# Optimization experiments

Measured on AMD Instinct MI355X. Metric: run time of the kernel, lower is better.

Reference implementation:

```python
import jax, jax.numpy as jnp
import numpy as np

B, S, D, H = 2, 1024, 2048, 16
NOPE, ROPE, VD, KVR, QLR = 128, 64, 128, 512, 1536
NE, TOPK, MI, SMI = 16, 2, 1408, 2816
QKD = NOPE + ROPE
SCALE = QKD ** -0.5
EPS = 1e-3


def _rms(x, w):
    return w * (x * jax.lax.rsqrt(jnp.mean(x * x, axis=-1, keepdims=True) + EPS))


def _lin(x, w, b):
    return x @ w.T + b


def _rope(x, cos, sin):
    # x: (B,S,H,dr); cos/sin: (S, dr//2); consecutive-pair complex rotation as in torch view_as_complex
    xs = x.reshape(*x.shape[:-1], -1, 2)
    x0, x1 = xs[..., 0], xs[..., 1]
    c = cos[None, :, None, :]
    s = sin[None, :, None, :]
    y = jnp.stack([x0 * c - x1 * s, x0 * s + x1 * c], axis=-1)
    return y.reshape(x.shape)


def setup_inputs() -> dict:
    ks = iter(jax.random.split(jax.random.key(0), 64))

    def w(*shape):
        return jax.random.normal(next(ks), shape, jnp.float32) * 0.02

    ang = jnp.arange(S)[:, None] * (1.0 / (10000.0 ** (jnp.arange(0, ROPE, 2) / ROPE)))[None, :]
    return {
        "x": jax.random.normal(next(ks), (B, S, D), jnp.float32),
        "attn_norm_w": jnp.ones(D, jnp.float32),
        "ffn_norm_w": jnp.ones(D, jnp.float32),
        "wq_a_w": w(QLR, D), "wq_a_b": w(QLR),
        "q_norm_w": jnp.ones(QLR, jnp.float32),
        "wq_b_w": w(H * QKD, QLR), "wq_b_b": w(H * QKD),
        "wkv_a_w": w(KVR + ROPE, D), "wkv_a_b": w(KVR + ROPE),
        "kv_norm_w": jnp.ones(KVR, jnp.float32),
        "wkv_b_w": w(H * (NOPE + VD), KVR),
        "wo_w": w(D, H * VD), "wo_b": w(D),
        "gate_w": w(NE, D), "gate_b": w(NE),
        "e_w1": w(NE, MI, D), "e_b1": w(NE, MI),
        "e_w2": w(NE, D, MI), "e_b2": w(NE, D),
        "e_w3": w(NE, MI, D), "e_b3": w(NE, MI),
        "s_w1": w(SMI, D), "s_b1": w(SMI),
        "s_w2": w(D, SMI), "s_b2": w(D),
        "s_w3": w(SMI, D), "s_b3": w(SMI),
        "cos": jnp.cos(ang), "sin": jnp.sin(ang),
        "start_pos": 0,
    }


def _forward(x, attn_norm_w, ffn_norm_w, wq_a_w, wq_a_b, q_norm_w, wq_b_w, wq_b_b,
             wkv_a_w, wkv_a_b, kv_norm_w, wkv_b_w, wo_w, wo_b,
             gate_w, gate_b, e_w1, e_b1, e_w2, e_b2, e_w3, e_b3,
             s_w1, s_b1, s_w2, s_b2, s_w3, s_b3, cos, sin, start_pos):
    # ---------------- MLA attention ----------------
    h = _rms(x, attn_norm_w)
    q = _lin(_rms(_lin(h, wq_a_w, wq_a_b), q_norm_w), wq_b_w, wq_b_b).reshape(B, S, H, QKD)
    q_nope, q_pe = q[..., :NOPE], q[..., NOPE:]
    q_pe = _rope(q_pe, cos, sin)
    kvf = _lin(h, wkv_a_w, wkv_a_b)
    kv, k_pe = kvf[..., :KVR], kvf[..., KVR:]
    k_pe = _rope(k_pe[:, :, None, :], cos, sin)[:, :, 0, :]          # (B,S,ROPE)
    wb = wkv_b_w.reshape(H, NOPE + VD, KVR)
    q_abs = jnp.einsum('bshd,hdc->bshc', q_nope, wb[:, :NOPE])       # absorbed q (B,S,H,KVR)
    kv_n = _rms(kv, kv_norm_w)                                       # kv cache content, start_pos=0
    scores = (jnp.einsum('bshc,btc->bsht', q_abs, kv_n)
              + jnp.einsum('bshr,btr->bsht', q_pe, k_pe)) * SCALE
    # NOTE: source constructs a causal mask but never applies it -> full attention (faithful)
    p = jax.nn.softmax(scores.astype(jnp.float32), axis=-1).astype(x.dtype)
    o = jnp.einsum('bsht,btc->bshc', p, kv_n)
    o = jnp.einsum('bshc,hdc->bshd', o, wb[:, NOPE:])
    x = x + _lin(o.reshape(B, S, H * VD), wo_w, wo_b)
    # ---------------- MoE FFN ----------------
    h2 = _rms(x, ffn_norm_w).reshape(-1, D)                          # (T,D)
    probs = jax.nn.softmax((h2 @ gate_w.T + gate_b).astype(jnp.float32), axis=-1)
    _, idx = jax.lax.top_k(probs + gate_b, TOPK)                     # bias re-added post-softmax, as in source
    wts = jnp.take_along_axis(probs, idx, axis=-1).astype(x.dtype)   # route_scale = 1.0
    T = h2.shape[0]
    combine = jnp.zeros((T, NE), x.dtype).at[jnp.arange(T)[:, None], idx].add(wts)
    a = jnp.einsum('td,eid->tei', h2, e_w1) + e_b1
    g = jax.nn.silu(a) * (jnp.einsum('td,eid->tei', h2, e_w3) + e_b3)
    gm = g * combine[:, :, None]
    y = jnp.einsum('tei,edi->td', gm, e_w2) + combine @ e_b2
    z = _lin(jax.nn.silu(_lin(h2, s_w1, s_b1)) * _lin(h2, s_w3, s_b3), s_w2, s_b2)
    return x + (y + z + h2).reshape(B, S, D)


def reference(x, attn_norm_w, ffn_norm_w, wq_a_w, wq_a_b, q_norm_w, wq_b_w, wq_b_b,
              wkv_a_w, wkv_a_b, kv_norm_w, wkv_b_w, wo_w, wo_b,
              gate_w, gate_b, e_w1, e_b1, e_w2, e_b2, e_w3, e_b3,
              s_w1, s_b1, s_w2, s_b2, s_w3, s_b3, cos, sin, start_pos):
    return _forward(x, attn_norm_w, ffn_norm_w, wq_a_w, wq_a_b, q_norm_w, wq_b_w, wq_b_b,
                    wkv_a_w, wkv_a_b, kv_norm_w, wkv_b_w, wo_w, wo_b,
                    gate_w, gate_b, e_w1, e_b1, e_w2, e_b2, e_w3, e_b3,
                    s_w1, s_b1, s_w2, s_b2, s_w3, s_b3, cos, sin, start_pos)
```

## Files before the change

### kernel.cpp

```cpp
#include <hip/hip_runtime.h>
#include <math.h>

constexpr int B_ = 2, S_ = 1024, D_ = 2048, H_ = 16;
constexpr int NOPE_ = 128, ROPE_ = 64, VD_ = 128, KVR_ = 512, QLR_ = 1536;
constexpr int NE_ = 16, MI_ = 1408, SMI_ = 2816;
constexpr int QKD_ = NOPE_ + ROPE_;
constexpr int T_ = B_ * S_;
constexpr float SCALE_ = 0.07216878364870322f;
constexpr float EPS_ = 1e-3f;
constexpr int MAX_TILES_ = 80;

typedef __attribute__((ext_vector_type(8))) short  bf16x8_t;
typedef __attribute__((ext_vector_type(4))) float  f32x4_t;
typedef __attribute__((ext_vector_type(4))) unsigned short us4_t;

__device__ __forceinline__ void split_bf(float v, unsigned short& h, unsigned short& l)
{
    unsigned int u = __float_as_uint(v);
    unsigned short hb = (unsigned short)((u + 0x7FFFu + ((u >> 16) & 1u)) >> 16);
    float hf = __uint_as_float((unsigned int)hb << 16);
    float lo = v - hf;
    unsigned int u2 = __float_as_uint(lo);
    l = (unsigned short)((u2 + 0x7FFFu + ((u2 >> 16) & 1u)) >> 16);
    h = hb;
}

__global__ __launch_bounds__(256) void gemm_mfma_kernel(
    const float* __restrict__ A, int lda, long strideA,
    const float* __restrict__ W, int ldw, long strideW, int w_kn,
    const float* __restrict__ bias, long strideBias,
    const float* __restrict__ res, int ldr, long strideRes,
    float* __restrict__ C, int ldc, long strideC,
    int M, int N, int K)
{
    (void)M; (void)N;
    const int bz = blockIdx.z;
    A += (long)bz * strideA;
    W += (long)bz * strideW;
    C += (long)bz * strideC;
    if (bias) bias += (long)bz * strideBias;
    if (res)  res  += (long)bz * strideRes;

    __shared__ unsigned short Ah[128][40], Al[128][40];
    __shared__ unsigned short Bh[128][40], Bl[128][40];

    const int m0 = blockIdx.y * 128;
    const int n0 = blockIdx.x * 128;
    const int tid  = threadIdx.x;
    const int lane = tid & 63;
    const int wv   = tid >> 6;
    const int wm = (wv >> 1) * 64, wn = (wv & 1) * 64;
    const int r16 = lane & 15, g4 = lane >> 4;

    f32x4_t acc[4][4];
    #pragma unroll
    for (int i = 0; i < 4; i++)
        #pragma unroll
        for (int j = 0; j < 4; j++) acc[i][j] = (f32x4_t){0.f, 0.f, 0.f, 0.f};

    const int sr   = tid >> 3;
    const int scol = (tid & 7) * 4;
    const int tcol = tid & 63, tkr = tid >> 6;

    for (int kt = 0; kt < K; kt += 32) {
        #pragma unroll
        for (int rr = 0; rr < 128; rr += 32) {
            const float4 v = *(const float4*)(A + (long)(m0 + rr + sr) * lda + (kt + scol));
            us4_t h, l;
            split_bf(v.x, ((unsigned short*)&h)[0], ((unsigned short*)&l)[0]);
            split_bf(v.y, ((unsigned short*)&h)[1], ((unsigned short*)&l)[1]);
            split_bf(v.z, ((unsigned short*)&h)[2], ((unsigned short*)&l)[2]);
            split_bf(v.w, ((unsigned short*)&h)[3], ((unsigned short*)&l)[3]);
            *(us4_t*)&Ah[rr + sr][scol] = h;
            *(us4_t*)&Al[rr + sr][scol] = l;
        }
        if (w_kn == 0) {
            #pragma unroll
            for (int rr = 0; rr < 128; rr += 32) {
                const float4 v = *(const float4*)(W + (long)(n0 + rr + sr) * ldw + (kt + scol));
                us4_t h, l;
                split_bf(v.x, ((unsigned short*)&h)[0], ((unsigned short*)&l)[0]);
                split_bf(v.y, ((unsigned short*)&h)[1], ((unsigned short*)&l)[1]);
                split_bf(v.z, ((unsigned short*)&h)[2], ((unsigned short*)&l)[2]);
                split_bf(v.w, ((unsigned short*)&h)[3], ((unsigned short*)&l)[3]);
                *(us4_t*)&Bh[rr + sr][scol] = h;
                *(us4_t*)&Bl[rr + sr][scol] = l;
            }
        } else {
            #pragma unroll
            for (int cb = 0; cb < 128; cb += 64)
                #pragma unroll
                for (int kb = 0; kb < 32; kb += 4) {
                    float v = W[(long)(kt + kb + tkr) * ldw + (n0 + cb + tcol)];
                    unsigned short h, l;
                    split_bf(v, h, l);
                    Bh[cb + tcol][kb + tkr] = h;
                    Bl[cb + tcol][kb + tkr] = l;
                }
        }
        __syncthreads();

        bf16x8_t ah[4], al[4], bh[4], bl[4];
        #pragma unroll
        for (int i = 0; i < 4; i++) {
            ah[i] = *(const bf16x8_t*)&Ah[wm + i * 16 + r16][g4 * 8];
            al[i] = *(const bf16x8_t*)&Al[wm + i * 16 + r16][g4 * 8];
            bh[i] = *(const bf16x8_t*)&Bh[wn + i * 16 + r16][g4 * 8];
            bl[i] = *(const bf16x8_t*)&Bl[wn + i * 16 + r16][g4 * 8];
        }
        #pragma unroll
        for (int i = 0; i < 4; i++)
            #pragma unroll
            for (int j = 0; j < 4; j++) {
                f32x4_t t = acc[i][j];
                t = __builtin_amdgcn_mfma_f32_16x16x32_bf16(ah[i], bh[j], t, 0, 0, 0);
                t = __builtin_amdgcn_mfma_f32_16x16x32_bf16(ah[i], bl[j], t, 0, 0, 0);
                t = __builtin_amdgcn_mfma_f32_16x16x32_bf16(al[i], bh[j], t, 0, 0, 0);
                acc[i][j] = t;
            }
        __syncthreads();
    }

    #pragma unroll
    for (int i = 0; i < 4; i++)
        #pragma unroll
        for (int rr = 0; rr < 4; rr++) {
            const int m = m0 + wm + i * 16 + g4 * 4 + rr;
            #pragma unroll
            for (int j = 0; j < 4; j++) {
                const int n = n0 + wn + j * 16 + r16;
                float v = acc[i][j][rr];
                if (bias) v += bias[n];
                if (res)  v += res[(long)m * ldr + n];
                C[(long)m * ldc + n] = v;
            }
        }
}

__global__ __launch_bounds__(256) void gemm_kernel(
    const float* __restrict__ A, int lda, long strideA,
    const float* __restrict__ W, int ldw, long strideW, int w_kn,
    const float* __restrict__ bias, long strideBias,
    const float* __restrict__ res, int ldr, long strideRes,
    float* __restrict__ C, int ldc, long strideC,
    int M, int N, int K)
{
    (void)M;
    const int bz = blockIdx.z;
    A += (long)bz * strideA;
    W += (long)bz * strideW;
    C += (long)bz * strideC;
    if (bias) bias += (long)bz * strideBias;
    if (res)  res  += (long)bz * strideRes;

    __shared__ float As[16][68];
    __shared__ float Ws[16][68];

    const int m0 = blockIdx.y * 64;
    const int n0 = blockIdx.x * 64;
    const int tid = threadIdx.x;
    const int tx = tid & 15;
    const int ty = tid >> 4;

    float acc[4][4] = {};

    for (int kt = 0; kt < K; kt += 16) {
        #pragma unroll
        for (int i = 0; i < 4; i++) {
            int p = tid + i * 256;
            int r = p >> 4, kk = p & 15;
            As[kk][r] = A[(long)(m0 + r) * lda + (kt + kk)];
        }
        if (w_kn) {
            #pragma unroll
            for (int i = 0; i < 4; i++) {
                int p = tid + i * 256;
                int kk = p >> 6, n = p & 63;
                Ws[kk][n] = W[(long)(kt + kk) * ldw + (n0 + n)];
            }
        } else {
            #pragma unroll
            for (int i = 0; i < 4; i++) {
                int p = tid + i * 256;
                int n = p >> 4, kk = p & 15;
                Ws[kk][n] = W[(long)(n0 + n) * ldw + (kt + kk)];
            }
        }
        __syncthreads();
        #pragma unroll
        for (int kk = 0; kk < 16; kk++) {
            float a[4], b[4];
            #pragma unroll
            for (int i = 0; i < 4; i++) a[i] = As[kk][ty * 4 + i];
            #pragma unroll
            for (int j = 0; j < 4; j++) b[j] = Ws[kk][tx * 4 + j];
            #pragma unroll
            for (int i = 0; i < 4; i++)
                #pragma unroll
                for (int j = 0; j < 4; j++)
                    acc[i][j] += a[i] * b[j];
        }
        __syncthreads();
    }

    #pragma unroll
    for (int i = 0; i < 4; i++) {
        int m = m0 + ty * 4 + i;
        #pragma unroll
        for (int j = 0; j < 4; j++) {
            int n = n0 + tx * 4 + j;
            float v = acc[i][j];
            if (bias) v += bias[n];
            if (res)  v += res[(long)m * ldr + n];
            C[(long)m * ldc + n] = v;
        }
    }
}

__global__ __launch_bounds__(256) void rms_kernel(
    const float* __restrict__ in, float* __restrict__ out,
    const float* __restrict__ w, int N, int in_stride, int out_stride)
{
    const int row = blockIdx.x;
    const float* x = in + (long)row * in_stride;
    float* y = out + (long)row * out_stride;
    __shared__ float red[256];
    const int tid = threadIdx.x;
    float s = 0.f;
    for (int i = tid; i < N; i += 256) { float v = x[i]; s += v * v; }
    red[tid] = s; __syncthreads();
    for (int st = 128; st > 0; st >>= 1) {
        if (tid < st) red[tid] += red[tid + st];
        __syncthreads();
    }
    const float scale = rsqrtf(red[0] / (float)N + EPS_);
    for (int i = tid; i < N; i += 256) y[i] = w[i] * x[i] * scale;
}

__global__ void rope_kernel(float* __restrict__ p,
                            const float* __restrict__ cosb,
                            const float* __restrict__ sinb,
                            int nheads, int row_stride, int head_stride,
                            int off, int total)
{
    int i = blockIdx.x * 256 + threadIdx.x;
    if (i >= total) return;
    int pair = i & 31;
    int rem = i >> 5;
    int h = rem % nheads;
    int t = rem / nheads;
    int s = t % S_;
    float c = cosb[s * 32 + pair], sn = sinb[s * 32 + pair];
    float* base = p + (long)t * row_stride + (long)h * head_stride + off + pair * 2;
    float x0 = base[0], x1 = base[1];
    base[0] = x0 * c - x1 * sn;
    base[1] = x0 * sn + x1 * c;
}

__global__ __launch_bounds__(256) void softmax_kernel(float* __restrict__ sc)
{
    float* row = sc + (long)blockIdx.x * 1024;
    const int tid = threadIdx.x;
    __shared__ float red[256];

    float4 v = ((const float4*)row)[tid];
    v.x *= SCALE_; v.y *= SCALE_; v.z *= SCALE_; v.w *= SCALE_;

    float m = fmaxf(fmaxf(v.x, v.y), fmaxf(v.z, v.w));
    red[tid] = m; __syncthreads();
    for (int st = 128; st > 0; st >>= 1) {
        if (tid < st) red[tid] = fmaxf(red[tid], red[tid + st]);
        __syncthreads();
    }
    m = red[0];
    __syncthreads();

    v.x = __expf(v.x - m); v.y = __expf(v.y - m);
    v.z = __expf(v.z - m); v.w = __expf(v.w - m);
    float s = v.x + v.y + v.z + v.w;
    red[tid] = s; __syncthreads();
    for (int st = 128; st > 0; st >>= 1) {
        if (tid < st) red[tid] += red[tid + st];
        __syncthreads();
    }
    const float inv = 1.f / red[0];

    v.x *= inv; v.y *= inv; v.z *= inv; v.w *= inv;
    ((float4*)row)[tid] = v;
}

__global__ __launch_bounds__(256) void gate_kernel(
    const float* __restrict__ h2, const float* __restrict__ gw,
    const float* __restrict__ gb, int* __restrict__ idx,
    float* __restrict__ wts)
{
    const int t = blockIdx.x;
    __shared__ float red[256];
    __shared__ float logits[16];
    const int tid = threadIdx.x;
    const int e = tid >> 4, lane = tid & 15;
    const float* x = h2 + (long)t * 2048;
    float s = 0.f;
    for (int i = lane; i < 2048; i += 16) s += x[i] * gw[e * 2048 + i];
    red[tid] = s; __syncthreads();
    for (int st = 8; st > 0; st >>= 1) {
        if (lane < st) red[tid] += red[tid + st];
        __syncthreads();
    }
    if (lane == 0) logits[e] = red[e * 16] + gb[e];
    __syncthreads();
    if (tid == 0) {
        float m = logits[0];
        for (int j = 1; j < 16; j++) m = fmaxf(m, logits[j]);
        float pr[16]; float sum = 0.f;
        for (int j = 0; j < 16; j++) { pr[j] = expf(logits[j] - m); sum += pr[j]; }
        float inv = 1.f / sum;
        for (int j = 0; j < 16; j++) pr[j] *= inv;
        int i1 = 0; float v1 = -1e30f;
        for (int j = 0; j < 16; j++) { float v = pr[j] + gb[j]; if (v > v1) { v1 = v; i1 = j; } }
        int i2 = 0; float v2 = -1e30f;
        for (int j = 0; j < 16; j++) { if (j == i1) continue; float v = pr[j] + gb[j]; if (v > v2) { v2 = v; i2 = j; } }
        idx[t * 2 + 0] = i1; idx[t * 2 + 1] = i2;
        wts[t * 2 + 0] = pr[i1]; wts[t * 2 + 1] = pr[i2];
    }
}

__global__ __launch_bounds__(256) void route_kernel(
    const int* __restrict__ idx, const float* __restrict__ wts,
    int* __restrict__ slot_te, float* __restrict__ slot_w,
    int* __restrict__ tile_e, int* __restrict__ tile_row0,
    int* __restrict__ tile_cnt, int* __restrict__ n_tiles)
{
    __shared__ int counts[16], offs[16], cursor[16];
    const int tid = threadIdx.x;
    if (tid < 16) { counts[tid] = 0; cursor[tid] = 0; }
    __syncthreads();
    for (int a = tid; a < 2 * T_; a += 256) atomicAdd(&counts[idx[a]], 1);
    __syncthreads();
    if (tid == 0) {
        int o = 0;
        for (int e = 0; e < 16; e++) { offs[e] = o; o += counts[e]; }
        int nt = 0;
        for (int e = 0; e < 16; e++) {
            for (int r0 = 0; r0 < counts[e]; r0 += 64) {
                tile_e[nt] = e;
                tile_row0[nt] = offs[e] + r0;
                int c = counts[e] - r0;
                tile_cnt[nt] = c < 64 ? c : 64;
                nt++;
            }
        }
        *n_tiles = nt;
    }
    __syncthreads();
    for (int a = tid; a < 2 * T_; a += 256) {
        int e = idx[a];
        int pos = offs[e] + atomicAdd(&cursor[e], 1);
        int t = a >> 1, k = a & 1;
        slot_te[pos * 2 + 0] = (t << 1) | k;
        slot_te[pos * 2 + 1] = e;
        slot_w[pos] = wts[a];
    }
}

__global__ __launch_bounds__(256) void moe_mlp13_kernel(
    const float* __restrict__ h2,
    const int* __restrict__ slot_te,
    const int* __restrict__ tile_e, const int* __restrict__ tile_row0,
    const int* __restrict__ tile_cnt, const int* __restrict__ n_tiles,
    const float* __restrict__ w1, const float* __restrict__ b1,
    const float* __restrict__ w3, const float* __restrict__ b3,
    float* __restrict__ G)
{
    const int tile = blockIdx.y;
    if (tile >= *n_tiles) return;
    const int e    = tile_e[tile];
    const int row0 = tile_row0[tile];
    const int tcnt = tile_cnt[tile];
    const int n0   = blockIdx.x * 128;

    __shared__ unsigned short Ah[64][40],  Al[64][40];
    __shared__ unsigned short B1h[128][40], B1l[128][40];
    __shared__ unsigned short B3h[128][40], B3l[128][40];
    __shared__ int tok[64];

    const int tid  = threadIdx.x;
    const int lane = tid & 63;
    const int wv   = tid >> 6;
    const int r16 = lane & 15, g4 = lane >> 4;

    if (tid < 64) {
        int r = tid < tcnt ? tid : tcnt - 1;
        tok[tid] = slot_te[(row0 + r) * 2 + 0] >> 1;
    }
    __syncthreads();

    const float* W1 = w1 + (long)e * MI_ * 2048;
    const float* W3 = w3 + (long)e * MI_ * 2048;

    f32x4_t acc1[4][2], acc3[4][2];
    #pragma unroll
    for (int i = 0; i < 4; i++)
        #pragma unroll
        for (int j = 0; j < 2; j++) {
            acc1[i][j] = (f32x4_t){0.f, 0.f, 0.f, 0.f};
            acc3[i][j] = (f32x4_t){0.f, 0.f, 0.f, 0.f};
        }

    const int sr   = tid >> 3;
    const int scol = (tid & 7) * 4;

    for (int kt = 0; kt < 2048; kt += 32) {
        #pragma unroll
        for (int rr = 0; rr < 64; rr += 32) {
            const float4 v = *(const float4*)(h2 + (long)tok[rr + sr] * 2048 + (kt + scol));
            us4_t h, l;
            split_bf(v.x, ((unsigned short*)&h)[0], ((unsigned short*)&l)[0]);
            split_bf(v.y, ((unsigned short*)&h)[1], ((unsigned short*)&l)[1]);
            split_bf(v.z, ((unsigned short*)&h)[2], ((unsigned short*)&l)[2]);
            split_bf(v.w, ((unsigned short*)&h)[3], ((unsigned short*)&l)[3]);
            *(us4_t*)&Ah[rr + sr][scol] = h;
            *(us4_t*)&Al[rr + sr][scol] = l;
        }
        #pragma unroll
        for (int rr = 0; rr < 128; rr += 32) {
            const long woff = (long)(n0 + rr + sr) * 2048 + (kt + scol);
            {
                const float4 v = *(const float4*)(W1 + woff);
                us4_t h, l;
                split_bf(v.x, ((unsigned short*)&h)[0], ((unsigned short*)&l)[0]);
                split_bf(v.y, ((unsigned short*)&h)[1], ((unsigned short*)&l)[1]);
                split_bf(v.z, ((unsigned short*)&h)[2], ((unsigned short*)&l)[2]);
                split_bf(v.w, ((unsigned short*)&h)[3], ((unsigned short*)&l)[3]);
                *(us4_t*)&B1h[rr + sr][scol] = h;
                *(us4_t*)&B1l[rr + sr][scol] = l;
            }
            {
                const float4 v = *(const float4*)(W3 + woff);
                us4_t h, l;
                split_bf(v.x, ((unsigned short*)&h)[0], ((unsigned short*)&l)[0]);
                split_bf(v.y, ((unsigned short*)&h)[1], ((unsigned short*)&l)[1]);
                split_bf(v.z, ((unsigned short*)&h)[2], ((unsigned short*)&l)[2]);
                split_bf(v.w, ((unsigned short*)&h)[3], ((unsigned short*)&l)[3]);
                *(us4_t*)&B3h[rr + sr][scol] = h;
                *(us4_t*)&B3l[rr + sr][scol] = l;
            }
        }
        __syncthreads();

        bf16x8_t ah[4], al[4], b1h[2], b1l[2], b3h[2], b3l[2];
        #pragma unroll
        for (int i = 0; i < 4; i++) {
            ah[i] = *(const bf16x8_t*)&Ah[i * 16 + r16][g4 * 8];
            al[i] = *(const bf16x8_t*)&Al[i * 16 + r16][g4 * 8];
        }
        #pragma unroll
        for (int j = 0; j < 2; j++) {
            const int cn = wv * 32 + j * 16 + r16;
            b1h[j] = *(const bf16x8_t*)&B1h[cn][g4 * 8];
            b1l[j] = *(const bf16x8_t*)&B1l[cn][g4 * 8];
            b3h[j] = *(const bf16x8_t*)&B3h[cn][g4 * 8];
            b3l[j] = *(const bf16x8_t*)&B3l[cn][g4 * 8];
        }
        #pragma unroll
        for (int i = 0; i < 4; i++)
            #pragma unroll
            for (int j = 0; j < 2; j++) {
                f32x4_t t = acc1[i][j];
                t = __builtin_amdgcn_mfma_f32_16x16x32_bf16(ah[i], b1h[j], t, 0, 0, 0);
                t = __builtin_amdgcn_mfma_f32_16x16x32_bf16(ah[i], b1l[j], t, 0, 0, 0);
                t = __builtin_amdgcn_mfma_f32_16x16x32_bf16(al[i], b1h[j], t, 0, 0, 0);
                acc1[i][j] = t;
                f32x4_t u = acc3[i][j];
                u = __builtin_amdgcn_mfma_f32_16x16x32_bf16(ah[i], b3h[j], u, 0, 0, 0);
                u = __builtin_amdgcn_mfma_f32_16x16x32_bf16(ah[i], b3l[j], u, 0, 0, 0);
                u = __builtin_amdgcn_mfma_f32_16x16x32_bf16(al[i], b3h[j], u, 0, 0, 0);
                acc3[i][j] = u;
            }
        __syncthreads();
    }

    #pragma unroll
    for (int i = 0; i < 4; i++)
        #pragma unroll
        for (int rr = 0; rr < 4; rr++) {
            const int rl = i * 16 + g4 * 4 + rr;
            if (rl >= tcnt) continue;
            const long grow = (long)(row0 + rl) * MI_;
            #pragma unroll
            for (int j = 0; j < 2; j++) {
                const int n = n0 + wv * 32 + j * 16 + r16;
                float a = acc1[i][j][rr] + b1[e * MI_ + n];
                float b = acc3[i][j][rr] + b3[e * MI_ + n];
                G[grow + n] = (a / (1.f + expf(-a))) * b;
            }
        }
}

__global__ __launch_bounds__(256) void moe_mlp2_kernel(
    const float* __restrict__ G,
    const int* __restrict__ slot_te, const float* __restrict__ slot_w,
    const int* __restrict__ tile_e, const int* __restrict__ tile_row0,
    const int* __restrict__ tile_cnt, const int* __restrict__ n_tiles,
    const float* __restrict__ w2, const float* __restrict__ b2,
    float* __restrict__ y0, float* __restrict__ y1)
{
    const int tile = blockIdx.y;
    if (tile >= *n_tiles) return;
    const int e    = tile_e[tile];
    const int row0 = tile_row0[tile];
    const int tcnt = tile_cnt[tile];
    const int n0   = blockIdx.x * 128;

    __shared__ unsigned short Ah[64][40], Al[64][40];
    __shared__ unsigned short Bh[128][40], Bl[128][40];
    __shared__ int rsrc[64];

    const int tid  = threadIdx.x;
    const int lane = tid & 63;
    const int wv   = tid >> 6;
    const int r16 = lane & 15, g4 = lane >> 4;

    if (tid < 64) {
        int r = tid < tcnt ? tid : tcnt - 1;
        rsrc[tid] = row0 + r;
    }
    __syncthreads();

    const float* W2 = w2 + (long)e * 2048 * MI_;

    f32x4_t acc[4][2];
    #pragma unroll
    for (int i = 0; i < 4; i++)
        #pragma unroll
        for (int j = 0; j < 2; j++) acc[i][j] = (f32x4_t){0.f, 0.f, 0.f, 0.f};

    const int sr   = tid >> 3;
    const int scol = (tid & 7) * 4;

    for (int kt = 0; kt < MI_; kt += 32) {
        #pragma unroll
        for (int rr = 0; rr < 64; rr += 32) {
            const float4 v = *(const float4*)(G + (long)rsrc[rr + sr] * MI_ + (kt + scol));
            us4_t h, l;
            split_bf(v.x, ((unsigned short*)&h)[0], ((unsigned short*)&l)[0]);
            split_bf(v.y, ((unsigned short*)&h)[1], ((unsigned short*)&l)[1]);
            split_bf(v.z, ((unsigned short*)&h)[2], ((unsigned short*)&l)[2]);
            split_bf(v.w, ((unsigned short*)&h)[3], ((unsigned short*)&l)[3]);
            *(us4_t*)&Ah[rr + sr][scol] = h;
            *(us4_t*)&Al[rr + sr][scol] = l;
        }
        #pragma unroll
        for (int rr = 0; rr < 128; rr += 32) {
            const float4 v = *(const float4*)(W2 + (long)(n0 + rr + sr) * MI_ + (kt + scol));
            us4_t h, l;
            split_bf(v.x, ((unsigned short*)&h)[0], ((unsigned short*)&l)[0]);
            split_bf(v.y, ((unsigned short*)&h)[1], ((unsigned short*)&l)[1]);
            split_bf(v.z, ((unsigned short*)&h)[2], ((unsigned short*)&l)[2]);
            split_bf(v.w, ((unsigned short*)&h)[3], ((unsigned short*)&l)[3]);
            *(us4_t*)&Bh[rr + sr][scol] = h;
            *(us4_t*)&Bl[rr + sr][scol] = l;
        }
        __syncthreads();

        bf16x8_t ah[4], al[4], bh[2], bl[2];
        #pragma unroll
        for (int i = 0; i < 4; i++) {
            ah[i] = *(const bf16x8_t*)&Ah[i * 16 + r16][g4 * 8];
            al[i] = *(const bf16x8_t*)&Al[i * 16 + r16][g4 * 8];
        }
        #pragma unroll
        for (int j = 0; j < 2; j++) {
            const int cn = wv * 32 + j * 16 + r16;
            bh[j] = *(const bf16x8_t*)&Bh[cn][g4 * 8];
            bl[j] = *(const bf16x8_t*)&Bl[cn][g4 * 8];
        }
        #pragma unroll
        for (int i = 0; i < 4; i++)
            #pragma unroll
            for (int j = 0; j < 2; j++) {
                f32x4_t t = acc[i][j];
                t = __builtin_amdgcn_mfma_f32_16x16x32_bf16(ah[i], bh[j], t, 0, 0, 0);
                t = __builtin_amdgcn_mfma_f32_16x16x32_bf16(ah[i], bl[j], t, 0, 0, 0);
                t = __builtin_amdgcn_mfma_f32_16x16x32_bf16(al[i], bh[j], t, 0, 0, 0);
                acc[i][j] = t;
            }
        __syncthreads();
    }

    #pragma unroll
    for (int i = 0; i < 4; i++)
        #pragma unroll
        for (int rr = 0; rr < 4; rr++) {
            const int rl = i * 16 + g4 * 4 + rr;
            if (rl >= tcnt) continue;
            const int slot = row0 + rl;
            const int tk = slot_te[slot * 2 + 0];
            const int t = tk >> 1, k = tk & 1;
            const float wgt = slot_w[slot];
            float* y = (k ? y1 : y0) + (long)t * 2048;
            #pragma unroll
            for (int j = 0; j < 2; j++) {
                const int n = n0 + wv * 32 + j * 16 + r16;
                y[n] = wgt * (acc[i][j][rr] + b2[e * 2048 + n]);
            }
        }
}

__global__ void silu_mul_kernel(float* __restrict__ u1,
                                const float* __restrict__ u3, long n)
{
    long i = (long)blockIdx.x * 256 + threadIdx.x;
    if (i >= n) return;
    float a = u1[i];
    u1[i] = (a / (1.f + expf(-a))) * u3[i];
}

__global__ void final_add_kernel(const float* __restrict__ x2,
                                 const float* __restrict__ h2,
                                 const float* __restrict__ y0,
                                 const float* __restrict__ y1,
                                 const float* __restrict__ z,
                                 float* __restrict__ out, long n)
{
    long i = (long)blockIdx.x * 256 + threadIdx.x;
    if (i >= n) return;
    out[i] = x2[i] + h2[i] + y0[i] + y1[i] + z[i];
}

extern "C" void kernel_launch(void* const* d_in, const int* in_sizes, int n_in,
                              void* d_out, int out_size, void* d_ws, size_t ws_size,
                              hipStream_t stream)
{
    (void)in_sizes; (void)n_in; (void)out_size; (void)ws_size;

    const float* x          = (const float*)d_in[0];
    const float* attn_nw    = (const float*)d_in[1];
    const float* ffn_nw     = (const float*)d_in[2];
    const float* wq_a_w     = (const float*)d_in[3];
    const float* wq_a_b     = (const float*)d_in[4];
    const float* q_norm_w   = (const float*)d_in[5];
    const float* wq_b_w     = (const float*)d_in[6];
    const float* wq_b_b     = (const float*)d_in[7];
    const float* wkv_a_w    = (const float*)d_in[8];
    const float* wkv_a_b    = (const float*)d_in[9];
    const float* kv_norm_w  = (const float*)d_in[10];
    const float* wkv_b_w    = (const float*)d_in[11];
    const float* wo_w       = (const float*)d_in[12];
    const float* wo_b       = (const float*)d_in[13];
    const float* gate_w     = (const float*)d_in[14];
    const float* gate_b     = (const float*)d_in[15];
    const float* e_w1       = (const float*)d_in[16];
    const float* e_b1       = (const float*)d_in[17];
    const float* e_w2       = (const float*)d_in[18];
    const float* e_b2       = (const float*)d_in[19];
    const float* e_w3       = (const float*)d_in[20];
    const float* e_b3       = (const float*)d_in[21];
    const float* s_w1       = (const float*)d_in[22];
    const float* s_b1       = (const float*)d_in[23];
    const float* s_w2       = (const float*)d_in[24];
    const float* s_b2       = (const float*)d_in[25];
    const float* s_w3       = (const float*)d_in[26];
    const float* s_b3       = (const float*)d_in[27];
    const float* cosb       = (const float*)d_in[28];
    const float* sinb       = (const float*)d_in[29];

    float* ws = (float*)d_ws;
    float* h    = ws + 0;
    float* qa   = ws + 4194304;
    float* q    = ws + 7340032;
    float* kvf  = ws + 13631488;
    float* qabs = ws + 14811136;
    float* o2   = ws + 31588352;
    float* x2   = ws + 35782656;
    float* h2   = ws + 39976960;
    float* u1   = ws + 44171264;
    float* u3   = ws + 49938432;
    float* wts  = ws + 55705600;
    int*   idx  = (int*)(ws + 55709696);
    int*   slot_te = (int*)(ws + 55713792);
    float* slot_w  = ws + 55721984;
    float* y0 = h;
    float* y1 = q;
    float* z  = u3;

    float* scores = o2;

    float* G = qabs;
    int* tile_e    = (int*)(qabs + 5767168);
    int* tile_row0 = tile_e + MAX_TILES_;
    int* tile_cnt  = tile_e + 2 * MAX_TILES_;
    int* n_tiles   = tile_e + 3 * MAX_TILES_;

    rms_kernel<<<dim3(T_), 256, 0, stream>>>(x, h, attn_nw, 2048, 2048, 2048);

    gemm_mfma_kernel<<<dim3(QLR_ / 128, T_ / 128, 1), 256, 0, stream>>>(
        h, 2048, 0, wq_a_w, 2048, 0, 0, wq_a_b, 0,
        nullptr, 0, 0, qa, QLR_, 0, T_, QLR_, 2048);

    rms_kernel<<<dim3(T_), 256, 0, stream>>>(qa, qa, q_norm_w, QLR_, QLR_, QLR_);

    gemm_mfma_kernel<<<dim3(H_ * QKD_ / 128, T_ / 128, 1), 256, 0, stream>>>(
        qa, QLR_, 0, wq_b_w, QLR_, 0, 0, wq_b_b, 0,
        nullptr, 0, 0, q, H_ * QKD_, 0, T_, H_ * QKD_, QLR_);

    gemm_kernel<<<dim3((KVR_ + ROPE_) / 64, T_ / 64, 1), 256, 0, stream>>>(
        h, 2048, 0, wkv_a_w, 2048, 0, 0, wkv_a_b, 0,
        nullptr, 0, 0, kvf, KVR_ + ROPE_, 0, T_, KVR_ + ROPE_, 2048);

    {
        int total_q = T_ * H_ * 32;
        rope_kernel<<<dim3((total_q + 255) / 256), 256, 0, stream>>>(
            q, cosb, sinb, H_, H_ * QKD_, QKD_, NOPE_, total_q);
        int total_k = T_ * 32;
        rope_kernel<<<dim3((total_k + 255) / 256), 256, 0, stream>>>(
            kvf, cosb, sinb, 1, KVR_ + ROPE_, 0, KVR_, total_k);
    }

    rms_kernel<<<dim3(T_), 256, 0, stream>>>(kvf, kvf, kv_norm_w, KVR_,
                                             KVR_ + ROPE_, KVR_ + ROPE_);

    gemm_mfma_kernel<<<dim3(KVR_ / 128, T_ / 128, H_), 256, 0, stream>>>(
        q, H_ * QKD_, QKD_,
        wkv_b_w, KVR_, (long)256 * KVR_, 1,
        nullptr, 0, nullptr, 0, 0,
        qabs, H_ * KVR_, KVR_, T_, KVR_, NOPE_);

    for (int b = 0; b < B_; b++) {
        const float* kvb = kvf + (long)b * S_ * (KVR_ + ROPE_);
        gemm_mfma_kernel<<<dim3(S_ / 128, S_ / 128, H_), 256, 0, stream>>>(
            qabs + (long)b * S_ * H_ * KVR_, H_ * KVR_, KVR_,
            kvb, KVR_ + ROPE_, 0, 0,
            nullptr, 0, nullptr, 0, 0,
            scores, S_, (long)S_ * S_, S_, S_, KVR_);
        gemm_mfma_kernel<<<dim3(S_ / 128, S_ / 128, H_), 256, 0, stream>>>(
            q + (long)b * S_ * H_ * QKD_ + NOPE_, H_ * QKD_, QKD_,
            kvb + KVR_, KVR_ + ROPE_, 0, 0,
            nullptr, 0, scores, S_, (long)S_ * S_,
            scores, S_, (long)S_ * S_, S_, S_, ROPE_);
        softmax_kernel<<<dim3(H_ * S_), 256, 0, stream>>>(scores);
        gemm_mfma_kernel<<<dim3(KVR_ / 128, S_ / 128, H_), 256, 0, stream>>>(
            scores, S_, (long)S_ * S_,
            kvb, KVR_ + ROPE_, 0, 1,
            nullptr, 0, nullptr, 0, 0,
            qabs + (long)b * S_ * H_ * KVR_, H_ * KVR_, KVR_, S_, KVR_, S_);
    }

    gemm_mfma_kernel<<<dim3(VD_ / 128, T_ / 128, H_), 256, 0, stream>>>(
        qabs, H_ * KVR_, KVR_,
        wkv_b_w + (long)NOPE_ * KVR_, KVR_, (long)256 * KVR_, 0,
        nullptr, 0, nullptr, 0, 0,
        o2, H_ * VD_, VD_, T_, VD_, KVR_);

    gemm_mfma_kernel<<<dim3(D_ / 128, T_ / 128, 1), 256, 0, stream>>>(
        o2, 2048, 0, wo_w, 2048, 0, 0, wo_b, 0,
        x, 2048, 0, x2, 2048, 0, T_, D_, 2048);

    rms_kernel<<<dim3(T_), 256, 0, stream>>>(x2, h2, ffn_nw, 2048, 2048, 2048);

    gate_kernel<<<dim3(T_), 256, 0, stream>>>(h2, gate_w, gate_b, idx, wts);

    route_kernel<<<dim3(1), 256, 0, stream>>>(idx, wts, slot_te, slot_w,
                                              tile_e, tile_row0, tile_cnt, n_tiles);

    moe_mlp13_kernel<<<dim3(MI_ / 128, MAX_TILES_), 256, 0, stream>>>(
        h2, slot_te, tile_e, tile_row0, tile_cnt, n_tiles,
        e_w1, e_b1, e_w3, e_b3, G);
    moe_mlp2_kernel<<<dim3(D_ / 128, MAX_TILES_), 256, 0, stream>>>(
        G, slot_te, slot_w, tile_e, tile_row0, tile_cnt, n_tiles,
        e_w2, e_b2, y0, y1);

    gemm_mfma_kernel<<<dim3(SMI_ / 128, T_ / 128, 1), 256, 0, stream>>>(
        h2, 2048, 0, s_w1, 2048, 0, 0, s_b1, 0,
        nullptr, 0, 0, u1, SMI_, 0, T_, SMI_, 2048);
    gemm_mfma_kernel<<<dim3(SMI_ / 128, T_ / 128, 1), 256, 0, stream>>>(
        h2, 2048, 0, s_w3, 2048, 0, 0, s_b3, 0,
        nullptr, 0, 0, u3, SMI_, 0, T_, SMI_, 2048);
    {
        long n = (long)T_ * SMI_;
        silu_mul_kernel<<<dim3((unsigned)((n + 255) / 256)), 256, 0, stream>>>(u1, u3, n);
    }
    gemm_mfma_kernel<<<dim3(D_ / 128, T_ / 128, 1), 256, 0, stream>>>(
        u1, SMI_, 0, s_w2, SMI_, 0, 0, s_b2, 0,
        nullptr, 0, 0, z, D_, 0, T_, D_, SMI_);

    {
        long n = (long)T_ * D_;
        final_add_kernel<<<dim3((unsigned)((n + 255) / 256)), 256, 0, stream>>>(
            x2, h2, y0, y1, z, (float*)d_out, n);
    }
}
```

Measured before the change: 2.740 ms.

## Fuse rope-score GEMM, silu-mul epilogue, MFMA kv_a GEMM, truncating bf16 split

Adds a second K-segment (A2/W2) to the MFMA GEMM so the nope and rope score products are computed in one launch instead of a separate accumulate pass. The silu-mul elementwise kernel is folded into the w3 GEMM epilogue, and the wkv_a projection moves from the scalar fp32 GEMM to the MFMA kernel with an N-limit clamp. The bf16 hi/lo split now truncates instead of rounding to nearest, which cuts ALU work during staging at some precision cost in the split-bf16 emulation.

```diff
diff --git a/kernel.cpp b/kernel.cpp
--- a/kernel.cpp
+++ b/kernel.cpp
@@ -17,27 +17,52 @@
 __device__ __forceinline__ void split_bf(float v, unsigned short& h, unsigned short& l)
 {
     unsigned int u = __float_as_uint(v);
-    unsigned short hb = (unsigned short)((u + 0x7FFFu + ((u >> 16) & 1u)) >> 16);
-    float hf = __uint_as_float((unsigned int)hb << 16);
-    float lo = v - hf;
-    unsigned int u2 = __float_as_uint(lo);
-    l = (unsigned short)((u2 + 0x7FFFu + ((u2 >> 16) & 1u)) >> 16);
-    h = hb;
+    h = (unsigned short)(u >> 16);
+    float lo = v - __uint_as_float(u & 0xFFFF0000u);
+    l = (unsigned short)(__float_as_uint(lo) >> 16);
+}
+
+__device__ __forceinline__ void split4(const float4& v, us4_t& h, us4_t& l)
+{
+    split_bf(v.x, ((unsigned short*)&h)[0], ((unsigned short*)&l)[0]);
+    split_bf(v.y, ((unsigned short*)&h)[1], ((unsigned short*)&l)[1]);
+    split_bf(v.z, ((unsigned short*)&h)[2], ((unsigned short*)&l)[2]);
+    split_bf(v.w, ((unsigned short*)&h)[3], ((unsigned short*)&l)[3]);
+}
+
+__device__ __forceinline__ void stage_rows(
+    const float* __restrict__ P, int ldp, int row0, int rowclamp,
+    int kt, int sr, int scol,
+    unsigned short (*__restrict__ Hs)[40], unsigned short (*__restrict__ Ls)[40])
+{
+    #pragma unroll
+    for (int rr = 0; rr < 128; rr += 32) {
+        int row = row0 + rr + sr;
+        if (row > rowclamp) row = rowclamp;
+        const float4 v = *(const float4*)(P + (long)row * ldp + (kt + scol));
+        us4_t h, l;
+        split4(v, h, l);
+        *(us4_t*)&Hs[rr + sr][scol] = h;
+        *(us4_t*)&Ls[rr + sr][scol] = l;
+    }
 }
 
 __global__ __launch_bounds__(256) void gemm_mfma_kernel(
     const float* __restrict__ A, int lda, long strideA,
     const float* __restrict__ W, int ldw, long strideW, int w_kn,
+    const float* __restrict__ A2, int lda2, long strideA2,
+    const float* __restrict__ W2, int ldw2, long strideW2, int K2,
     const float* __restrict__ bias, long strideBias,
-    const float* __restrict__ res, int ldr, long strideRes,
+    const float* __restrict__ res, int ldr, long strideRes, int res_mode,
     float* __restrict__ C, int ldc, long strideC,
-    int M, int N, int K)
-{
-    (void)M; (void)N;
+    int Nlim, int K)
+{
     const int bz = blockIdx.z;
     A += (long)bz * strideA;
     W += (long)bz * strideW;
     C += (long)bz * strideC;
+    if (A2)   A2  += (long)bz * strideA2;
+    if (W2)   W2  += (long)bz * strideW2;
     if (bias) bias += (long)bz * strideBias;
     if (res)  res  += (long)bz * strideRes;
 
@@ -63,29 +88,9 @@
     const int tcol = tid & 63, tkr = tid >> 6;
 
     for (int kt = 0; kt < K; kt += 32) {
-        #pragma unroll
-        for (int rr = 0; rr < 128; rr += 32) {
-            const float4 v = *(const float4*)(A + (long)(m0 + rr + sr) * lda + (kt + scol));
-            us4_t h, l;
-            split_bf(v.x, ((unsigned short*)&h)[0], ((unsigned short*)&l)[0]);
-            split_bf(v.y, ((unsigned short*)&h)[1], ((unsigned short*)&l)[1]);
-            split_bf(v.z, ((unsigned short*)&h)[2], ((unsigned short*)&l)[2]);
-            split_bf(v.w, ((unsigned short*)&h)[3], ((unsigned short*)&l)[3]);
-            *(us4_t*)&Ah[rr + sr][scol] = h;
-            *(us4_t*)&Al[rr + sr][scol] = l;
-        }
+        stage_rows(A, lda, m0, 1 << 30, kt, sr, scol, Ah, Al);
         if (w_kn == 0) {
-            #pragma unroll
-            for (int rr = 0; rr < 128; rr += 32) {
-                const float4 v = *(const float4*)(W + (long)(n0 + rr + sr) * ldw + (kt + scol));
-                us4_t h, l;
-                split_bf(v.x, ((unsigned short*)&h)[0], ((unsigned short*)&l)[0]);
-                split_bf(v.y, ((unsigned short*)&h)[1], ((unsigned short*)&l)[1]);
-                split_bf(v.z, ((unsigned short*)&h)[2], ((unsigned short*)&l)[2]);
-                split_bf(v.w, ((unsigned short*)&h)[3], ((unsigned short*)&l)[3]);
-                *(us4_t*)&Bh[rr + sr][scol] = h;
-                *(us4_t*)&Bl[rr + sr][scol] = l;
-            }
+            stage_rows(W, ldw, n0, Nlim - 1, kt, sr, scol, Bh, Bl);
         } else {
             #pragma unroll
             for (int cb = 0; cb < 128; cb += 64)
@@ -121,6 +126,33 @@
         __syncthreads();
     }
 
+    if (K2 > 0) {
+        for (int kt = 0; kt < K2; kt += 32) {
+            stage_rows(A2, lda2, m0, 1 << 30, kt, sr, scol, Ah, Al);
+            stage_rows(W2, ldw2, n0, Nlim - 1, kt, sr, scol, Bh, Bl);
+            __syncthreads();
+            bf16x8_t ah[4], al[4], bh[4], bl[4];
+            #pragma unroll
+            for (int i = 0; i < 4; i++) {
+                ah[i] = *(const bf16x8_t*)&Ah[wm + i * 16 + r16][g4 * 8];
+                al[i] = *(const bf16x8_t*)&Al[wm + i * 16 + r16][g4 * 8];
+                bh[i] = *(const bf16x8_t*)&Bh[wn + i * 16 + r16][g4 * 8];
+                bl[i] = *(const bf16x8_t*)&Bl[wn + i * 16 + r16][g4 * 8];
+            }
+            #pragma unroll
+            for (int i = 0; i < 4; i++)
+                #pragma unroll
+                for (int j = 0; j < 4; j++) {
+                    f32x4_t t = acc[i][j];
+                    t = __builtin_amdgcn_mfma_f32_16x16x32_bf16(ah[i], bh[j], t, 0, 0, 0);
+                    t = __builtin_amdgcn_mfma_f32_16x16x32_bf16(ah[i], bl[j], t, 0, 0, 0);
+                    t = __builtin_amdgcn_mfma_f32_16x16x32_bf16(al[i], bh[j], t, 0, 0, 0);
+                    acc[i][j] = t;
+                }
+            __syncthreads();
+        }
+    }
+
     #pragma unroll
     for (int i = 0; i < 4; i++)
         #pragma unroll
@@ -129,92 +161,18 @@
             #pragma unroll
             for (int j = 0; j < 4; j++) {
                 const int n = n0 + wn + j * 16 + r16;
+                if (n >= Nlim) continue;
                 float v = acc[i][j][rr];
                 if (bias) v += bias[n];
-                if (res)  v += res[(long)m * ldr + n];
+                if (res_mode == 1) {
+                    v += res[(long)m * ldr + n];
+                } else if (res_mode == 2) {
+                    float r = res[(long)m * ldr + n];
+                    v = (r / (1.f + expf(-r))) * v;
+                }
                 C[(long)m * ldc + n] = v;
             }
         }
-}
-
-__global__ __launch_bounds__(256) void gemm_kernel(
-    const float* __restrict__ A, int lda, long strideA,
-    const float* __restrict__ W, int ldw, long strideW, int w_kn,
-    const float* __restrict__ bias, long strideBias,
-    const float* __restrict__ res, int ldr, long strideRes,
-    float* __restrict__ C, int ldc, long strideC,
-    int M, int N, int K)
-{
-    (void)M;
-    const int bz = blockIdx.z;
-    A += (long)bz * strideA;
-    W += (long)bz * strideW;
-    C += (long)bz * strideC;
-    if (bias) bias += (long)bz * strideBias;
-    if (res)  res  += (long)bz * strideRes;
-
-    __shared__ float As[16][68];
-    __shared__ float Ws[16][68];
-
-    const int m0 = blockIdx.y * 64;
-    const int n0 = blockIdx.x * 64;
-    const int tid = threadIdx.x;
-    const int tx = tid & 15;
-    const int ty = tid >> 4;
-
-    float acc[4][4] = {};
-
-    for (int kt = 0; kt < K; kt += 16) {
-        #pragma unroll
-        for (int i = 0; i < 4; i++) {
-            int p = tid + i * 256;
-            int r = p >> 4, kk = p & 15;
-            As[kk][r] = A[(long)(m0 + r) * lda + (kt + kk)];
-        }
-        if (w_kn) {
-            #pragma unroll
-            for (int i = 0; i < 4; i++) {
-                int p = tid + i * 256;
-                int kk = p >> 6, n = p & 63;
-                Ws[kk][n] = W[(long)(kt + kk) * ldw + (n0 + n)];
-            }
-        } else {
-            #pragma unroll
-            for (int i = 0; i < 4; i++) {
-                int p = tid + i * 256;
-                int n = p >> 4, kk = p & 15;
-                Ws[kk][n] = W[(long)(n0 + n) * ldw + (kt + kk)];
-            }
-        }
-        __syncthreads();
-        #pragma unroll
-        for (int kk = 0; kk < 16; kk++) {
-            float a[4], b[4];
-            #pragma unroll
-            for (int i = 0; i < 4; i++) a[i] = As[kk][ty * 4 + i];
-            #pragma unroll
-            for (int j = 0; j < 4; j++) b[j] = Ws[kk][tx * 4 + j];
-            #pragma unroll
-            for (int i = 0; i < 4; i++)
-                #pragma unroll
-                for (int j = 0; j < 4; j++)
-                    acc[i][j] += a[i] * b[j];
-        }
-        __syncthreads();
-    }
-
-    #pragma unroll
-    for (int i = 0; i < 4; i++) {
-        int m = m0 + ty * 4 + i;
-        #pragma unroll
-        for (int j = 0; j < 4; j++) {
-            int n = n0 + tx * 4 + j;
-            float v = acc[i][j];
-            if (bias) v += bias[n];
-            if (res)  v += res[(long)m * ldr + n];
-            C[(long)m * ldc + n] = v;
-        }
-    }
 }
 
 __global__ __launch_bounds__(256) void rms_kernel(
@@ -415,10 +373,7 @@
         for (int rr = 0; rr < 64; rr += 32) {
             const float4 v = *(const float4*)(h2 + (long)tok[rr + sr] * 2048 + (kt + scol));
             us4_t h, l;
-            split_bf(v.x, ((unsigned short*)&h)[0], ((unsigned short*)&l)[0]);
-            split_bf(v.y, ((unsigned short*)&h)[1], ((unsigned short*)&l)[1]);
-            split_bf(v.z, ((unsigned short*)&h)[2], ((unsigned short*)&l)[2]);
-            split_bf(v.w, ((unsigned short*)&h)[3], ((unsigned short*)&l)[3]);
+            split4(v, h, l);
             *(us4_t*)&Ah[rr + sr][scol] = h;
             *(us4_t*)&Al[rr + sr][scol] = l;
         }
@@ -428,20 +383,14 @@
             {
                 const float4 v = *(const float4*)(W1 + woff);
                 us4_t h, l;
-                split_bf(v.x, ((unsigned short*)&h)[0], ((unsigned short*)&l)[0]);
-                split_bf(v.y, ((unsigned short*)&h)[1], ((unsigned short*)&l)[1]);
-                split_bf(v.z, ((unsigned short*)&h)[2], ((unsigned short*)&l)[2]);
-                split_bf(v.w, ((unsigned short*)&h)[3], ((unsigned short*)&l)[3]);
+                split4(v, h, l);
                 *(us4_t*)&B1h[rr + sr][scol] = h;
                 *(us4_t*)&B1l[rr + sr][scol] = l;
             }
             {
                 const float4 v = *(const float4*)(W3 + woff);
                 us4_t h, l;
-                split_bf(v.x, ((unsigned short*)&h)[0], ((unsigned short*)&l)[0]);
-                split_bf(v.y, ((unsigned short*)&h)[1], ((unsigned short*)&l)[1]);
-                split_bf(v.z, ((unsigned short*)&h)[2], ((unsigned short*)&l)[2]);
-                split_bf(v.w, ((unsigned short*)&h)[3], ((unsigned short*)&l)[3]);
+                split4(v, h, l);
                 *(us4_t*)&B3h[rr + sr][scol] = h;
                 *(us4_t*)&B3l[rr + sr][scol] = l;
             }
@@ -543,10 +492,7 @@
         for (int rr = 0; rr < 64; rr += 32) {
             const float4 v = *(const float4*)(G + (long)rsrc[rr + sr] * MI_ + (kt + scol));
             us4_t h, l;
-            split_bf(v.x, ((unsigned short*)&h)[0], ((unsigned short*)&l)[0]);
-            split_bf(v.y, ((unsigned short*)&h)[1], ((unsigned short*)&l)[1]);
-            split_bf(v.z, ((unsigned short*)&h)[2], ((unsigned short*)&l)[2]);
-            split_bf(v.w, ((unsigned short*)&h)[3], ((unsigned short*)&l)[3]);
+            split4(v, h, l);
             *(us4_t*)&Ah[rr + sr][scol] = h;
             *(us4_t*)&Al[rr + sr][scol] = l;
         }
@@ -554,10 +500,7 @@
         for (int rr = 0; rr < 128; rr += 32) {
             const float4 v = *(const float4*)(W2 + (long)(n0 + rr + sr) * MI_ + (kt + scol));
             us4_t h, l;
-            split_bf(v.x, ((unsigned short*)&h)[0], ((unsigned short*)&l)[0]);
-            split_bf(v.y, ((unsigned short*)&h)[1], ((unsigned short*)&l)[1]);
-            split_bf(v.z, ((unsigned short*)&h)[2], ((unsigned short*)&l)[2]);
-            split_bf(v.w, ((unsigned short*)&h)[3], ((unsigned short*)&l)[3]);
+            split4(v, h, l);
             *(us4_t*)&Bh[rr + sr][scol] = h;
             *(us4_t*)&Bl[rr + sr][scol] = l;
         }
@@ -605,15 +548,6 @@
                 y[n] = wgt * (acc[i][j][rr] + b2[e * 2048 + n]);
             }
         }
-}
-
-__global__ void silu_mul_kernel(float* __restrict__ u1,
-                                const float* __restrict__ u3, long n)
-{
-    long i = (long)blockIdx.x * 256 + threadIdx.x;
-    if (i >= n) return;
-    float a = u1[i];
-    u1[i] = (a / (1.f + expf(-a))) * u3[i];
 }
 
 __global__ void final_add_kernel(const float* __restrict__ x2,
@@ -695,18 +629,24 @@
     rms_kernel<<<dim3(T_), 256, 0, stream>>>(x, h, attn_nw, 2048, 2048, 2048);
 
     gemm_mfma_kernel<<<dim3(QLR_ / 128, T_ / 128, 1), 256, 0, stream>>>(
-        h, 2048, 0, wq_a_w, 2048, 0, 0, wq_a_b, 0,
-        nullptr, 0, 0, qa, QLR_, 0, T_, QLR_, 2048);
+        h, 2048, 0, wq_a_w, 2048, 0, 0,
+        nullptr, 0, 0, nullptr, 0, 0, 0,
+        wq_a_b, 0, nullptr, 0, 0, 0,
+        qa, QLR_, 0, QLR_, 2048);
 
     rms_kernel<<<dim3(T_), 256, 0, stream>>>(qa, qa, q_norm_w, QLR_, QLR_, QLR_);
 
     gemm_mfma_kernel<<<dim3(H_ * QKD_ / 128, T_ / 128, 1), 256, 0, stream>>>(
-        qa, QLR_, 0, wq_b_w, QLR_, 0, 0, wq_b_b, 0,
-        nullptr, 0, 0, q, H_ * QKD_, 0, T_, H_ * QKD_, QLR_);
-
-    gemm_kernel<<<dim3((KVR_ + ROPE_) / 64, T_ / 64, 1), 256, 0, stream>>>(
-        h, 2048, 0, wkv_a_w, 2048, 0, 0, wkv_a_b, 0,
-        nullptr, 0, 0, kvf, KVR_ + ROPE_, 0, T_, KVR_ + ROPE_, 2048);
+        qa, QLR_, 0, wq_b_w, QLR_, 0, 0,
+        nullptr, 0, 0, nullptr, 0, 0, 0,
+        wq_b_b, 0, nullptr, 0, 0, 0,
+        q, H_ * QKD_, 0, H_ * QKD_, QLR_);
+
+    gemm_mfma_kernel<<<dim3(5, T_ / 128, 1), 256, 0, stream>>>(
+        h, 2048, 0, wkv_a_w, 2048, 0, 0,
+        nullptr, 0, 0, nullptr, 0, 0, 0,
+        wkv_a_b, 0, nullptr, 0, 0, 0,
+        kvf, KVR_ + ROPE_, 0, KVR_ + ROPE_, 2048);
 
     {
         int total_q = T_ * H_ * 32;
@@ -723,38 +663,40 @@
     gemm_mfma_kernel<<<dim3(KVR_ / 128, T_ / 128, H_), 256, 0, stream>>>(
         q, H_ * QKD_, QKD_,
         wkv_b_w, KVR_, (long)256 * KVR_, 1,
-        nullptr, 0, nullptr, 0, 0,
-        qabs, H_ * KVR_, KVR_, T_, KVR_, NOPE_);
+        nullptr, 0, 0, nullptr, 0, 0, 0,
+        nullptr, 0, nullptr, 0, 0, 0,
+        qabs, H_ * KVR_, KVR_, KVR_, NOPE_);
 
     for (int b = 0; b < B_; b++) {
         const float* kvb = kvf + (long)b * S_ * (KVR_ + ROPE_);
         gemm_mfma_kernel<<<dim3(S_ / 128, S_ / 128, H_), 256, 0, stream>>>(
             qabs + (long)b * S_ * H_ * KVR_, H_ * KVR_, KVR_,
             kvb, KVR_ + ROPE_, 0, 0,
-            nullptr, 0, nullptr, 0, 0,
-            scores, S_, (long)S_ * S_, S_, S_, KVR_);
-        gemm_mfma_kernel<<<dim3(S_ / 128, S_ / 128, H_), 256, 0, stream>>>(
             q + (long)b * S_ * H_ * QKD_ + NOPE_, H_ * QKD_, QKD_,
-            kvb + KVR_, KVR_ + ROPE_, 0, 0,
-            nullptr, 0, scores, S_, (long)S_ * S_,
-            scores, S_, (long)S_ * S_, S_, S_, ROPE_);
+            kvb + KVR_, KVR_ + ROPE_, 0, ROPE_,
+            nullptr, 0, nullptr, 0, 0, 0,
+            scores, S_, (long)S_ * S_, S_, KVR_);
         softmax_kernel<<<dim3(H_ * S_), 256, 0, stream>>>(scores);
         gemm_mfma_kernel<<<dim3(KVR_ / 128, S_ / 128, H_), 256, 0, stream>>>(
             scores, S_, (long)S_ * S_,
             kvb, KVR_ + ROPE_, 0, 1,
-            nullptr, 0, nullptr, 0, 0,
-            qabs + (long)b * S_ * H_ * KVR_, H_ * KVR_, KVR_, S_, KVR_, S_);
+            nullptr, 0, 0, nullptr, 0, 0, 0,
+            nullptr, 0, nullptr, 0, 0, 0,
+            qabs + (long)b * S_ * H_ * KVR_, H_ * KVR_, KVR_, KVR_, S_);
     }
 
     gemm_mfma_kernel<<<dim3(VD_ / 128, T_ / 128, H_), 256, 0, stream>>>(
         qabs, H_ * KVR_, KVR_,
         wkv_b_w + (long)NOPE_ * KVR_, KVR_, (long)256 * KVR_, 0,
-        nullptr, 0, nullptr, 0, 0,
-        o2, H_ * VD_, VD_, T_, VD_, KVR_);
+        nullptr, 0, 0, nullptr, 0, 0, 0,
+        nullptr, 0, nullptr, 0, 0, 0,
+        o2, H_ * VD_, VD_, VD_, KVR_);
 
     gemm_mfma_kernel<<<dim3(D_ / 128, T_ / 128, 1), 256, 0, stream>>>(
-        o2, 2048, 0, wo_w, 2048, 0, 0, wo_b, 0,
-        x, 2048, 0, x2, 2048, 0, T_, D_, 2048);
+        o2, 2048, 0, wo_w, 2048, 0, 0,
+        nullptr, 0, 0, nullptr, 0, 0, 0,
+        wo_b, 0, x, 2048, 0, 1,
+        x2, 2048, 0, D_, 2048);
 
     rms_kernel<<<dim3(T_), 256, 0, stream>>>(x2, h2, ffn_nw, 2048, 2048, 2048);
 
@@ -771,18 +713,20 @@
         e_w2, e_b2, y0, y1);
 
     gemm_mfma_kernel<<<dim3(SMI_ / 128, T_ / 128, 1), 256, 0, stream>>>(
-        h2, 2048, 0, s_w1, 2048, 0, 0, s_b1, 0,
-        nullptr, 0, 0, u1, SMI_, 0, T_, SMI_, 2048);
+        h2, 2048, 0, s_w1, 2048, 0, 0,
+        nullptr, 0, 0, nullptr, 0, 0, 0,
+        s_b1, 0, nullptr, 0, 0, 0,
+        u1, SMI_, 0, SMI_, 2048);
     gemm_mfma_kernel<<<dim3(SMI_ / 128, T_ / 128, 1), 256, 0, stream>>>(
-        h2, 2048, 0, s_w3, 2048, 0, 0, s_b3, 0,
-        nullptr, 0, 0, u3, SMI_, 0, T_, SMI_, 2048);
-    {
-        long n = (long)T_ * SMI_;
-        silu_mul_kernel<<<dim3((unsigned)((n + 255) / 256)), 256, 0, stream>>>(u1, u3, n);
-    }
+        h2, 2048, 0, s_w3, 2048, 0, 0,
+        nullptr, 0, 0, nullptr, 0, 0, 0,
+        s_b3, 0, u1, SMI_, 0, 2,
+        u1, SMI_, 0, SMI_, 2048);
     gemm_mfma_kernel<<<dim3(D_ / 128, T_ / 128, 1), 256, 0, stream>>>(
-        u1, SMI_, 0, s_w2, SMI_, 0, 0, s_b2, 0,
-        nullptr, 0, 0, z, D_, 0, T_, D_, SMI_);
+        u1, SMI_, 0, s_w2, SMI_, 0, 0,
+        nullptr, 0, 0, nullptr, 0, 0, 0,
+        s_b2, 0, nullptr, 0, 0, 0,
+        z, D_, 0, D_, SMI_);
 
     {
         long n = (long)T_ * D_;
```

Measured after the change: 2.684 ms. 1.02x faster.
